# Performance work log

Hardware: AMD Instinct MI355X
Metric: run time of the kernel (lower is better)

## Reference

```python
import jax, jax.numpy as jnp
import numpy as np

EPS = 1e-5
LAMBDA_REG = 1.0
ALPHA_ENTROPY = 0.5
ALPHA_DIVERSITY = 0.5

B, N, D, K = 32, 1024, 256, 512  # batch, tokens, dim_embed, num_embed


def setup_inputs() -> dict:
    key = jax.random.key(0)
    k0, k1, k2 = jax.random.split(key, 3)
    inputs = jax.random.normal(k0, (B, N, D), dtype=jnp.float32)
    gamma = jnp.ones((D,), jnp.float32)
    beta = jnp.zeros((D,), jnp.float32)
    # keras 'uniform' initializer default: U(-0.05, 0.05)
    embed_w = jax.random.uniform(k1, (D, K), jnp.float32, -0.05, 0.05)
    # keras 'random_normal' default: stddev=0.05
    d_w = jax.random.normal(k2, (D, D), jnp.float32) * 0.05
    d_b = jnp.zeros((D,), jnp.float32)
    return {"inputs": inputs, "gamma": gamma, "beta": beta,
            "embed_w": embed_w, "d_w": d_w, "d_b": d_b}


def _project_columns_to_simplex(P_sol):
    # P_sol: (K, M); project each column onto the probability simplex.
    P_t = P_sol.T                                   # (M, K)
    sorted_P = -jnp.sort(-P_t, axis=1)              # descending
    cumsum = jnp.cumsum(sorted_P, axis=1)
    k = jnp.arange(1, K + 1, dtype=P_t.dtype)
    thresholds = (cumsum - 1.0) / k
    valid = (sorted_P > thresholds).astype(jnp.int32)
    max_idx = jnp.argmax(valid * jnp.arange(K, dtype=jnp.int32), axis=1)  # (M,)
    sel_cumsum = jnp.take_along_axis(cumsum, max_idx[:, None], axis=1)[:, 0]
    theta = (sel_cumsum - 1.0) / (max_idx.astype(P_t.dtype) + 1.0)
    return jax.nn.relu(P_t - theta[:, None]).T      # (K, M)


def _forward(inputs, gamma, beta, embed_w, d_w, d_b):
    # dense + layernorm
    x = jnp.matmul(inputs, d_w) + d_b
    mean = jnp.mean(x, axis=-1, keepdims=True)
    var = jnp.var(x, axis=-1, keepdims=True)
    x = gamma * ((x - mean) / jnp.sqrt(var + EPS)) + beta

    flat = x.reshape(-1, D)                          # (M, D)
    flat_sg = jax.lax.stop_gradient(flat)

    # hard assignment (VQ-style, on detached encodings)
    dists = (jnp.sum(flat_sg ** 2, axis=1, keepdims=True)
             + jnp.sum(embed_w ** 2, axis=0, keepdims=True)
             - 2.0 * jnp.matmul(flat_sg, embed_w))   # (M, K)
    assign = jnp.argmin(dists, axis=1)
    P_tilde = jax.nn.one_hot(assign, K, dtype=jnp.float32).T  # (K, M)

    # regularized least squares: (C^T C + lam I) P = C^T Z + lam P_tilde
    C = embed_w                                       # (D, K)
    Z = flat.T                                        # (D, M)
    A = jnp.matmul(C.T, C) + LAMBDA_REG * jnp.eye(K, dtype=jnp.float32)
    b = jnp.matmul(C.T, Z) + LAMBDA_REG * P_tilde     # (K, M)
    P_sol = jnp.linalg.solve(A, b)
    P_proj = _project_columns_to_simplex(P_sol)       # (K, M)

    out_P_proj = P_proj.T.reshape(B, N, K)

    # perplexity
    p_j = jnp.mean(out_P_proj, axis=(0, 1))
    p_j = jnp.clip(p_j, 1e-10, 1.0 - 1e-9)
    p_j = p_j / jnp.sum(p_j)
    entropy_bits = -jnp.sum(p_j * jnp.log(p_j) / jnp.log(2.0))
    perplexity = jnp.power(2.0, entropy_bits)

    Zq_flat = jnp.matmul(C, P_proj).T                 # (M, D)

    # entropy regularizer
    p_mean = jnp.mean(out_P_proj, axis=(0, 1))
    p_mn = p_mean / (jnp.sum(p_mean) + EPS)
    entropy_reg = -jnp.sum(p_mn * jnp.log(p_mn + EPS))

    # diversity loss on l2-normalized codebook columns
    norm_cb = embed_w / jnp.sqrt(jnp.maximum(jnp.sum(embed_w ** 2, axis=0, keepdims=True), 1e-12))
    sims = jnp.matmul(norm_cb.T, norm_cb)
    masked = sims * (1.0 - jnp.eye(K, dtype=jnp.float32))
    diversity_loss = jnp.mean(jax.nn.relu(masked))

    primary_loss = jnp.mean((Zq_flat - flat) ** 2)  # discrete_loss=False path
    loss = primary_loss + ALPHA_ENTROPY * entropy_reg + ALPHA_DIVERSITY * diversity_loss

    Zq = Zq_flat.reshape(B, N, D)
    return Zq, out_P_proj, loss, perplexity


def reference(inputs, gamma, beta, embed_w, d_w, d_b):
    return _forward(inputs, gamma, beta, embed_w, d_w, d_b)
```

## Files before the change

### kernel.cpp

```cpp
#include <hip/hip_runtime.h>
#include <math.h>


#define M_ 32768
#define D_ 256
#define K_ 512
#define TAU 0.006f

typedef short bf16x8 __attribute__((ext_vector_type(8)));
typedef unsigned short u16x8 __attribute__((ext_vector_type(8)));
typedef unsigned short u16x4 __attribute__((ext_vector_type(4)));
typedef float f32x4 __attribute__((ext_vector_type(4)));

#define LSTR 56

__device__ inline void split_rne(float f, unsigned short& h, unsigned short& l)
{
    unsigned int u = __float_as_uint(f);
    unsigned int uh = u + (0x7FFFu + ((u >> 16) & 1u));
    h = (unsigned short)(uh >> 16);
    float fh = __uint_as_float(((unsigned int)h) << 16);
    float r = f - fh;
    l = (unsigned short)(__float_as_uint(r) >> 16);
}

__device__ inline unsigned short rne16(float f)
{
    unsigned int u = __float_as_uint(f);
    u += 0x7FFFu + ((u >> 16) & 1u);
    return (unsigned short)(u >> 16);
}

template<int EPI>
__global__ __launch_bounds__(256)
void mfma_gemm(const unsigned short* __restrict__ Ah,
               const unsigned short* __restrict__ Bh,
               float* __restrict__ Out, int Kd, int N,
               const float* __restrict__ AinvM, const int* __restrict__ assign,
               const float* Zref, float* __restrict__ lossPart)
{
    __shared__ unsigned short sA[128*LSTR];
    __shared__ unsigned short sB[128*LSTR];
    __shared__ float red[256];
    const int tid = threadIdx.x;
    const int m0 = blockIdx.y * 128, n0 = blockIdx.x * 128;
    const int w = tid >> 6, lane = tid & 63;
    const int wr = (w & 1) * 64, wc = (w >> 1) * 64;
    const int cg = lane >> 4, cr = lane & 15;

    f32x4 acc[4][4];
    const f32x4 z4 = {0.f, 0.f, 0.f, 0.f};
#pragma unroll
    for (int i = 0; i < 4; ++i)
#pragma unroll
        for (int j = 0; j < 4; ++j) acc[i][j] = z4;

    const int sr = tid >> 1;
    const int sk = (tid & 1) * 16;
    const int soff = sr * LSTR + sk;
    const unsigned short* Agh = Ah + (size_t)(m0 + sr) * Kd + sk;
    const unsigned short* Bgh = Bh + (size_t)(n0 + sr) * Kd + sk;

    for (int kb = 0; kb < Kd; kb += 32) {
        *(u16x8*)&sA[soff]     = *(const u16x8*)(Agh + kb);
        *(u16x8*)&sA[soff + 8] = *(const u16x8*)(Agh + kb + 8);
        *(u16x8*)&sB[soff]     = *(const u16x8*)(Bgh + kb);
        *(u16x8*)&sB[soff + 8] = *(const u16x8*)(Bgh + kb + 8);
        __syncthreads();
        bf16x8 ah[4], bh[4];
#pragma unroll
        for (int f = 0; f < 4; ++f) {
            ah[f] = *(const bf16x8*)&sA[(wr + f*16 + cr) * LSTR + cg*8];
            bh[f] = *(const bf16x8*)&sB[(wc + f*16 + cr) * LSTR + cg*8];
        }
#pragma unroll
        for (int i = 0; i < 4; ++i)
#pragma unroll
            for (int j = 0; j < 4; ++j)
                acc[i][j] = __builtin_amdgcn_mfma_f32_16x16x32_bf16(ah[i], bh[j], acc[i][j], 0, 0, 0);
        __syncthreads();
    }

    if (EPI == 2) {
#pragma unroll
        for (int i = 0; i < 4; ++i) {
#pragma unroll
            for (int q = 0; q < 4; ++q) {
                const int row = m0 + wr + i*16 + cg*4 + q;
                const int am = assign[row];
                const float* Arow = AinvM + (size_t)am * K_ + n0 + wc;
#pragma unroll
                for (int j = 0; j < 4; ++j)
                    Out[(size_t)row * N + n0 + wc + j*16 + cr] =
                        acc[i][j][q] + Arow[j*16 + cr];
            }
        }
    } else {
        float lsum = 0.f;
#pragma unroll
        for (int i = 0; i < 4; ++i) {
#pragma unroll
            for (int q = 0; q < 4; ++q) {
                const int row = m0 + wr + i*16 + cg*4 + q;
#pragma unroll
                for (int j = 0; j < 4; ++j) {
                    const int col = n0 + wc + j*16 + cr;
                    const float v = acc[i][j][q];
                    const float zv = Zref[(size_t)row * N + col];
                    const float d = v - zv;
                    lsum += d * d;
                    Out[(size_t)row * N + col] = v;
                }
            }
        }
        red[tid] = lsum;
        __syncthreads();
        for (int s = 128; s > 0; s >>= 1) {
            if (tid < s) red[tid] += red[tid + s];
            __syncthreads();
        }
        if (tid == 0) lossPart[blockIdx.y * gridDim.x + blockIdx.x] = red[0];
    }
}

__global__ __launch_bounds__(256)
void score_mfma_argmin(const unsigned short* __restrict__ Zh, const unsigned short* __restrict__ Zl,
                       const unsigned short* __restrict__ Bth, const unsigned short* __restrict__ Btl,
                       const float* __restrict__ cn2, const float* __restrict__ zn2,
                       float* __restrict__ PV, float* __restrict__ PB,
                       int* __restrict__ PI)
{
    __shared__ unsigned short sAh[128*LSTR], sAl[128*LSTR];
    __shared__ unsigned short sBh[128*LSTR], sBl[128*LSTR];
    __shared__ float l1v[128][2], l2v[128][2];
    __shared__ int   liv[128][2];
    const int tid = threadIdx.x;
    const int m0 = blockIdx.y * 128, n0 = blockIdx.x * 128;
    const int w = tid >> 6, lane = tid & 63;
    const int wr = (w & 1) * 64, wc = (w >> 1) * 64;
    const int cg = lane >> 4, cr = lane & 15;

    f32x4 acc[4][4];
    const f32x4 z4 = {0.f, 0.f, 0.f, 0.f};
#pragma unroll
    for (int i = 0; i < 4; ++i)
#pragma unroll
        for (int j = 0; j < 4; ++j) acc[i][j] = z4;

    const int sr = tid >> 1;
    const int sk = (tid & 1) * 16;
    const int soff = sr * LSTR + sk;
    const unsigned short* Ah = Zh  + (size_t)(m0 + sr) * D_ + sk;
    const unsigned short* Al = Zl  + (size_t)(m0 + sr) * D_ + sk;
    const unsigned short* Bh = Bth + (size_t)(n0 + sr) * D_ + sk;
    const unsigned short* Bl = Btl + (size_t)(n0 + sr) * D_ + sk;

    for (int kb = 0; kb < D_; kb += 32) {
        *(u16x8*)&sAh[soff]     = *(const u16x8*)(Ah + kb);
        *(u16x8*)&sAh[soff + 8] = *(const u16x8*)(Ah + kb + 8);
        *(u16x8*)&sAl[soff]     = *(const u16x8*)(Al + kb);
        *(u16x8*)&sAl[soff + 8] = *(const u16x8*)(Al + kb + 8);
        *(u16x8*)&sBh[soff]     = *(const u16x8*)(Bh + kb);
        *(u16x8*)&sBh[soff + 8] = *(const u16x8*)(Bh + kb + 8);
        *(u16x8*)&sBl[soff]     = *(const u16x8*)(Bl + kb);
        *(u16x8*)&sBl[soff + 8] = *(const u16x8*)(Bl + kb + 8);
        __syncthreads();
        bf16x8 ah[4], al[4], bh[4], bl[4];
#pragma unroll
        for (int f = 0; f < 4; ++f) {
            const int ao = (wr + f*16 + cr) * LSTR + cg*8;
            ah[f] = *(const bf16x8*)&sAh[ao];
            al[f] = *(const bf16x8*)&sAl[ao];
            const int bo = (wc + f*16 + cr) * LSTR + cg*8;
            bh[f] = *(const bf16x8*)&sBh[bo];
            bl[f] = *(const bf16x8*)&sBl[bo];
        }
#pragma unroll
        for (int i = 0; i < 4; ++i)
#pragma unroll
            for (int j = 0; j < 4; ++j) {
                acc[i][j] = __builtin_amdgcn_mfma_f32_16x16x32_bf16(ah[i], bh[j], acc[i][j], 0, 0, 0);
                acc[i][j] = __builtin_amdgcn_mfma_f32_16x16x32_bf16(al[i], bh[j], acc[i][j], 0, 0, 0);
                acc[i][j] = __builtin_amdgcn_mfma_f32_16x16x32_bf16(ah[i], bl[j], acc[i][j], 0, 0, 0);
            }
        __syncthreads();
    }

    const int half = wc >> 6;
#pragma unroll
    for (int i = 0; i < 4; ++i) {
#pragma unroll
        for (int q = 0; q < 4; ++q) {
            const int rl = wr + i*16 + cg*4 + q;
            const float zr = zn2[m0 + rl];
            float b1 = 3.4e38f, b2 = 3.4e38f; int i1 = 0x7fffffff;
#pragma unroll
            for (int j = 0; j < 4; ++j) {
                const int col = n0 + wc + j*16 + cr;
                const float d = (zr + cn2[col]) - 2.0f * acc[i][j][q];
                if (d < b1 || (d == b1 && col < i1)) { b2 = b1; b1 = d; i1 = col; }
                else if (d < b2) b2 = d;
            }
#pragma unroll
            for (int off = 1; off < 16; off <<= 1) {
                const float o1 = __shfl_xor(b1, off);
                const int   oi = __shfl_xor(i1, off);
                const float o2 = __shfl_xor(b2, off);
                if (o1 < b1 || (o1 == b1 && oi < i1)) { b2 = fminf(b1, o2); b1 = o1; i1 = oi; }
                else { b2 = fminf(o1, b2); }
            }
            if (cr == 0) { l1v[rl][half] = b1; l2v[rl][half] = b2; liv[rl][half] = i1; }
        }
    }
    __syncthreads();
    if (tid < 128) {
        const float a1 = l1v[tid][0], a2 = l2v[tid][0]; const int ai = liv[tid][0];
        const float c1 = l1v[tid][1], c2 = l2v[tid][1]; const int ci = liv[tid][1];
        float b1, b2; int bi;
        if (c1 < a1 || (c1 == a1 && ci < ai)) { b1 = c1; bi = ci; b2 = fminf(a1, c2); }
        else { b1 = a1; bi = ai; b2 = fminf(c1, a2); }
        const size_t o = (size_t)(m0 + tid) * 4 + blockIdx.x;
        PV[o] = b1; PB[o] = b2; PI[o] = bi;
    }
}

__global__ void argmin_reduce4(const float* __restrict__ PV, const float* __restrict__ PB,
                               const int* __restrict__ PI, int* __restrict__ assign,
                               int* __restrict__ rlist, int* __restrict__ rcount)
{
    const int m = blockIdx.x * 256 + threadIdx.x;
    float b1 = PV[(size_t)m*4], b2 = PB[(size_t)m*4]; int i1 = PI[(size_t)m*4];
#pragma unroll
    for (int s = 1; s < 4; ++s) {
        const float o1 = PV[(size_t)m*4+s], o2 = PB[(size_t)m*4+s];
        const int oi = PI[(size_t)m*4+s];
        if (o1 < b1 || (o1 == b1 && oi < i1)) { b2 = fminf(b1, o2); b1 = o1; i1 = oi; }
        else { b2 = fminf(o1, b2); }
    }
    assign[m] = i1;
    if (b2 - b1 < TAU) { const int p = atomicAdd(rcount, 1); rlist[p] = m; }
}

__global__ __launch_bounds__(256)
void repair_gemm(const float* __restrict__ Z, const float* __restrict__ B,
                 const float* __restrict__ cn2, const float* __restrict__ zn2,
                 const int* __restrict__ rlist, const int* __restrict__ rcount,
                 float* __restrict__ PV, int* __restrict__ PI)
{
    const int n = rcount[0];
    const int m0 = blockIdx.y * 128;
    if (m0 >= n) return;
    __shared__ float As[16][132];
    __shared__ float Bs[16][128];
    __shared__ int rows_s[128];
    const int tid = threadIdx.x;
    const int tx = tid & 15, ty = tid >> 4;
    const int n0 = blockIdx.x * 128;

    if (tid < 128) rows_s[tid] = (m0 + tid < n) ? rlist[m0 + tid] : rlist[0];
    __syncthreads();

    float acc[8][8];
#pragma unroll
    for (int i = 0; i < 8; ++i)
#pragma unroll
        for (int j = 0; j < 8; ++j) acc[i][j] = 0.f;

    const int ar = tid >> 1, ac = (tid & 1) * 8;
    const int br = tid >> 4, bc = (tid & 15) * 8;
    const float* Ap = Z + (size_t)rows_s[ar] * D_ + ac;
    const float* Bp = B + (size_t)br * K_ + n0 + bc;

    for (int kb = 0; kb < D_; kb += 16) {
        float4 a0 = *(const float4*)(Ap + kb);
        float4 a1 = *(const float4*)(Ap + kb + 4);
        float4 b0 = *(const float4*)(Bp + (size_t)kb * K_);
        float4 b1 = *(const float4*)(Bp + (size_t)kb * K_ + 4);
        As[ac+0][ar] = a0.x; As[ac+1][ar] = a0.y; As[ac+2][ar] = a0.z; As[ac+3][ar] = a0.w;
        As[ac+4][ar] = a1.x; As[ac+5][ar] = a1.y; As[ac+6][ar] = a1.z; As[ac+7][ar] = a1.w;
        *(float4*)&Bs[br][bc]     = b0;
        *(float4*)&Bs[br][bc + 4] = b1;
        __syncthreads();
#pragma unroll
        for (int kk = 0; kk < 16; ++kk) {
            float4 av0 = *(const float4*)&As[kk][ty*4];
            float4 av1 = *(const float4*)&As[kk][64 + ty*4];
            float4 bv0 = *(const float4*)&Bs[kk][tx*4];
            float4 bv1 = *(const float4*)&Bs[kk][64 + tx*4];
            float a_[8] = {av0.x, av0.y, av0.z, av0.w, av1.x, av1.y, av1.z, av1.w};
            float b_[8] = {bv0.x, bv0.y, bv0.z, bv0.w, bv1.x, bv1.y, bv1.z, bv1.w};
#pragma unroll
            for (int i = 0; i < 8; ++i)
#pragma unroll
                for (int j = 0; j < 8; ++j)
                    acc[i][j] = fmaf(a_[i], b_[j], acc[i][j]);
        }
        __syncthreads();
    }

#pragma unroll
    for (int hi = 0; hi < 2; ++hi) {
#pragma unroll
        for (int i = 0; i < 4; ++i) {
            const int rl = hi*64 + ty*4 + i;
            if (m0 + rl >= n) continue;
            const float zr = zn2[rows_s[rl]];
            float best = 3.4e38f; int bi = 0x7fffffff;
#pragma unroll
            for (int hj = 0; hj < 2; ++hj) {
#pragma unroll
                for (int j = 0; j < 4; ++j) {
                    const int col = n0 + hj*64 + tx*4 + j;
                    const float t1 = zr + cn2[col];
                    const float d  = t1 - 2.0f * acc[hi*4+i][hj*4+j];
                    if (d < best) { best = d; bi = col; }
                }
            }
#pragma unroll
            for (int off = 1; off < 16; off <<= 1) {
                const float ov = __shfl_xor(best, off);
                const int   oi = __shfl_xor(bi, off);
                if (ov < best || (ov == best && oi < bi)) { best = ov; bi = oi; }
            }
            if (tx == 0) {
                PV[(size_t)(m0 + rl) * 4 + blockIdx.x] = best;
                PI[(size_t)(m0 + rl) * 4 + blockIdx.x] = bi;
            }
        }
    }
}

__global__ void repair_scatter(const float* __restrict__ PV, const int* __restrict__ PI,
                               const int* __restrict__ rlist, const int* __restrict__ rcount,
                               int* __restrict__ assign)
{
    const int r = blockIdx.x * 256 + threadIdx.x;
    if (r >= rcount[0]) return;
    float best = PV[(size_t)r * 4]; int bi = PI[(size_t)r * 4];
#pragma unroll
    for (int nb = 1; nb < 4; ++nb) {
        const float v = PV[(size_t)r * 4 + nb]; const int ix = PI[(size_t)r * 4 + nb];
        if (v < best || (v == best && ix < bi)) { best = v; bi = ix; }
    }
    assign[rlist[r]] = bi;
}

__global__ __launch_bounds__(512)
void dense_ln_kernel(const float* __restrict__ A, const float* __restrict__ Bw,
                     const float* __restrict__ bias, const float* __restrict__ gamma,
                     const float* __restrict__ beta, float* __restrict__ Z,
                     float* __restrict__ zn2,
                     unsigned short* __restrict__ Zh, unsigned short* __restrict__ Zl)
{
    __shared__ float As[16][68];
    __shared__ float Bs[16][260];
    __shared__ float rred[64][17];
    __shared__ float rstat[64];
    const int tid = threadIdx.x, tx = tid & 15, ty = tid >> 4;
    const int m0 = blockIdx.x * 64;
    float acc[2][16];
#pragma unroll
    for (int i = 0; i < 2; ++i)
#pragma unroll
        for (int j = 0; j < 16; ++j) acc[i][j] = 0.f;

    const int ar = tid >> 3, ac = (tid & 7) * 2;
    const int br = tid >> 5, bc = (tid & 31) * 8;
    for (int kb = 0; kb < 256; kb += 16) {
        {
            float2 a = *(const float2*)(A + (size_t)(m0 + ar) * 256 + kb + ac);
            As[ac][ar] = a.x; As[ac + 1][ar] = a.y;
            *(float4*)&Bs[br][bc]     = *(const float4*)(Bw + (size_t)(kb + br) * 256 + bc);
            *(float4*)&Bs[br][bc + 4] = *(const float4*)(Bw + (size_t)(kb + br) * 256 + bc + 4);
        }
        __syncthreads();
#pragma unroll
        for (int kk = 0; kk < 16; ++kk) {
            float av[2] = {As[kk][ty*2], As[kk][ty*2 + 1]};
            float bv[16];
#pragma unroll
            for (int q = 0; q < 4; ++q) {
                float4 b4 = *(const float4*)&Bs[kk][q*64 + tx*4];
                bv[q*4+0] = b4.x; bv[q*4+1] = b4.y; bv[q*4+2] = b4.z; bv[q*4+3] = b4.w;
            }
#pragma unroll
            for (int i = 0; i < 2; ++i)
#pragma unroll
                for (int j = 0; j < 16; ++j)
                    acc[i][j] = fmaf(av[i], bv[j], acc[i][j]);
        }
        __syncthreads();
    }

    float bcol[16];
#pragma unroll
    for (int q = 0; q < 4; ++q) {
        float4 b4 = *(const float4*)(bias + q*64 + tx*4);
        bcol[q*4+0] = b4.x; bcol[q*4+1] = b4.y; bcol[q*4+2] = b4.z; bcol[q*4+3] = b4.w;
    }
#pragma unroll
    for (int i = 0; i < 2; ++i)
#pragma unroll
        for (int j = 0; j < 16; ++j) acc[i][j] += bcol[j];

#pragma unroll
    for (int i = 0; i < 2; ++i) {
        float s = 0.f;
#pragma unroll
        for (int j = 0; j < 16; ++j) s += acc[i][j];
        rred[ty*2+i][tx] = s;
    }
    __syncthreads();
    if (tid < 64) {
        float s = 0.f;
#pragma unroll
        for (int t = 0; t < 16; ++t) s += rred[tid][t];
        rstat[tid] = s * (1.f / 256.f);
    }
    __syncthreads();
    float mean_[2];
#pragma unroll
    for (int i = 0; i < 2; ++i) mean_[i] = rstat[ty*2+i];

#pragma unroll
    for (int i = 0; i < 2; ++i) {
        float s = 0.f;
#pragma unroll
        for (int j = 0; j < 16; ++j) { float d = acc[i][j] - mean_[i]; s += d * d; }
        rred[ty*2+i][tx] = s;
    }
    __syncthreads();
    if (tid < 64) {
        float s = 0.f;
#pragma unroll
        for (int t = 0; t < 16; ++t) s += rred[tid][t];
        rstat[tid] = s * (1.f / 256.f);
    }
    __syncthreads();
    float rstd_[2];
#pragma unroll
    for (int i = 0; i < 2; ++i) rstd_[i] = sqrtf(rstat[ty*2+i] + 1e-5f);

    float gam[16], bet[16];
#pragma unroll
    for (int q = 0; q < 4; ++q) {
        float4 g4 = *(const float4*)(gamma + q*64 + tx*4);
        float4 e4 = *(const float4*)(beta  + q*64 + tx*4);
        gam[q*4+0] = g4.x; gam[q*4+1] = g4.y; gam[q*4+2] = g4.z; gam[q*4+3] = g4.w;
        bet[q*4+0] = e4.x; bet[q*4+1] = e4.y; bet[q*4+2] = e4.z; bet[q*4+3] = e4.w;
    }
#pragma unroll
    for (int i = 0; i < 2; ++i)
#pragma unroll
        for (int j = 0; j < 16; ++j) {
            const float d = acc[i][j] - mean_[i];
            acc[i][j] = gam[j] * (d / rstd_[i]) + bet[j];
        }

#pragma unroll
    for (int i = 0; i < 2; ++i) {
        float s = 0.f;
#pragma unroll
        for (int j = 0; j < 16; ++j) s += acc[i][j] * acc[i][j];
        rred[ty*2+i][tx] = s;
    }
    __syncthreads();
    if (tid < 64) {
        float s = 0.f;
#pragma unroll
        for (int t = 0; t < 16; ++t) s += rred[tid][t];
        zn2[m0 + tid] = s;
    }

#pragma unroll
    for (int i = 0; i < 2; ++i) {
        const int row = m0 + ty*2 + i;
#pragma unroll
        for (int q = 0; q < 4; ++q) {
            float4 v;
            v.x = acc[i][q*4+0]; v.y = acc[i][q*4+1];
            v.z = acc[i][q*4+2]; v.w = acc[i][q*4+3];
            const size_t pos = (size_t)row * 256 + q*64 + tx*4;
            *(float4*)(Z + pos) = v;
            unsigned short h[4], l[4];
            split_rne(v.x, h[0], l[0]); split_rne(v.y, h[1], l[1]);
            split_rne(v.z, h[2], l[2]); split_rne(v.w, h[3], l[3]);
            *(u16x4*)(Zh + pos) = *(u16x4*)h;
            *(u16x4*)(Zl + pos) = *(u16x4*)l;
        }
    }
}

template<int TRA, int ASUM, int BSUM, int OEPI>
__global__ __launch_bounds__(256)
void sk_gemm(const float* __restrict__ A, const float* __restrict__ B,
             float* __restrict__ Out, int M, int N, int Kd,
             const float* __restrict__ Xprev)
{
    __shared__ float As[16][68];
    __shared__ float Bs[16][68];
    const int tid = threadIdx.x;
    const int tx = tid & 15, ty = tid >> 4;
    const int n0 = blockIdx.x * 64, m0 = blockIdx.y * 64;
    const int kw = Kd >> 2;
    const int kb0 = blockIdx.z * kw;
    const size_t aP = (size_t)M * Kd;
    const size_t bP = (size_t)Kd * N;
    float acc[4][4];
#pragma unroll
    for (int i = 0; i < 4; ++i)
#pragma unroll
        for (int j = 0; j < 4; ++j) acc[i][j] = 0.f;

    for (int kb = kb0; kb < kb0 + kw; kb += 16) {
        if (TRA == 0) {
            const int ar2 = tid >> 2, ac2 = (tid & 3) * 4;
            const size_t off = (size_t)(m0 + ar2) * Kd + kb + ac2;
            float4 a;
            if (ASUM) {
                float4 a0 = *(const float4*)(A + off);
                float4 a1 = *(const float4*)(A + aP + off);
                float4 a2 = *(const float4*)(A + 2*aP + off);
                float4 a3 = *(const float4*)(A + 3*aP + off);
                a.x = a0.x + a1.x + a2.x + a3.x;
                a.y = a0.y + a1.y + a2.y + a3.y;
                a.z = a0.z + a1.z + a2.z + a3.z;
                a.w = a0.w + a1.w + a2.w + a3.w;
                if (ASUM == 2) {
                    const int row = m0 + ar2, colb = kb + ac2;
                    if (row == colb)     a.x += 1.f;
                    if (row == colb + 1) a.y += 1.f;
                    if (row == colb + 2) a.z += 1.f;
                    if (row == colb + 3) a.w += 1.f;
                }
            } else {
                a = *(const float4*)(A + off);
            }
            As[ac2+0][ar2] = a.x; As[ac2+1][ar2] = a.y;
            As[ac2+2][ar2] = a.z; As[ac2+3][ar2] = a.w;
        } else {
            const int ar2 = tid >> 4, ac2 = (tid & 15) * 4;
            float4 a = *(const float4*)(A + (size_t)(kb + ar2) * M + m0 + ac2);
            *(float4*)&As[ar2][ac2] = a;
        }
        {
            const int br2 = tid >> 4, bc2 = (tid & 15) * 4;
            const size_t off = (size_t)(kb + br2) * N + n0 + bc2;
            float4 b;
            if (BSUM) {
                float4 b0 = *(const float4*)(B + off);
                float4 b1 = *(const float4*)(B + bP + off);
                float4 b2 = *(const float4*)(B + 2*bP + off);
                float4 b3 = *(const float4*)(B + 3*bP + off);
                b.x = b0.x + b1.x + b2.x + b3.x;
                b.y = b0.y + b1.y + b2.y + b3.y;
                b.z = b0.z + b1.z + b2.z + b3.z;
                b.w = b0.w + b1.w + b2.w + b3.w;
            } else {
                b = *(const float4*)(B + off);
            }
            *(float4*)&Bs[br2][bc2] = b;
        }
        __syncthreads();
#pragma unroll
        for (int kk = 0; kk < 16; ++kk) {
            float4 a4 = *(const float4*)&As[kk][ty*4];
            float4 b4 = *(const float4*)&Bs[kk][tx*4];
            float a_[4] = {a4.x, a4.y, a4.z, a4.w};
            float b_[4] = {b4.x, b4.y, b4.z, b4.w};
#pragma unroll
            for (int i = 0; i < 4; ++i)
#pragma unroll
                for (int j = 0; j < 4; ++j)
                    acc[i][j] = fmaf(a_[i], b_[j], acc[i][j]);
        }
        __syncthreads();
    }
    const size_t MN = (size_t)M * N;
    float* Op = Out + (size_t)blockIdx.z * MN;
#pragma unroll
    for (int i = 0; i < 4; ++i)
#pragma unroll
        for (int j = 0; j < 4; ++j) {
            const size_t idx = (size_t)(m0 + ty*4 + i) * N + n0 + tx*4 + j;
            if (OEPI == 0) {
                Op[idx] = acc[i][j];
            } else {
                float base = 0.f;
                if (blockIdx.z == 0)
                    base = 2.f * (Xprev[idx] + Xprev[MN + idx] +
                                  Xprev[2*MN + idx] + Xprev[3*MN + idx]);
                Op[idx] = base - acc[i][j];
            }
        }
}

__global__ __launch_bounds__(256)
void prep_c(const float* __restrict__ C, float* __restrict__ Ct,
            unsigned short* __restrict__ Cth, unsigned short* __restrict__ Ctl,
            unsigned short* __restrict__ Ch, float* __restrict__ cn2,
            int* __restrict__ rcount)
{
    __shared__ float red[256];
    const int k = blockIdx.x, t = threadIdx.x;
    const float v = C[(size_t)t * K_ + k];
    Ct[k * 256 + t] = v;
    unsigned short h, l;
    split_rne(v, h, l);
    Cth[k * 256 + t] = h;
    Ctl[k * 256 + t] = l;
    Ch[(size_t)t * K_ + k] = h;
    red[t] = v * v;
    __syncthreads();
    for (int s = 128; s > 0; s >>= 1) { if (t < s) red[t] += red[t + s]; __syncthreads(); }
    if (t == 0) {
        cn2[k] = red[0];
        if (k == 0) rcount[0] = 0;
    }
}

__global__ void rowabs_kernel(const float* __restrict__ Sp, float* __restrict__ rowAbs)
{
    __shared__ float red[256];
    const int r = blockIdx.x, t = threadIdx.x;
    const int idx = r * 256 + t;
    float v = Sp[idx] + Sp[65536 + idx] + Sp[131072 + idx] + Sp[196608 + idx];
    if (r == t) v += 1.f;
    red[t] = fabsf(v); __syncthreads();
    for (int s = 128; s > 0; s >>= 1) {
        if (t < s) red[t] += red[t + s];
        __syncthreads();
    }
    if (t == 0) rowAbs[r] = red[0];
}

__global__ void x1_init(const float* __restrict__ rowAbs, const float* __restrict__ Sp,
                        float* __restrict__ Xp)
{
    __shared__ float red[256];
    const int t = threadIdx.x;
    red[t] = rowAbs[t]; __syncthreads();
    for (int s = 128; s > 0; s >>= 1) {
        if (t < s) red[t] = fmaxf(red[t], red[t + s]);
        __syncthreads();
    }
    const float c = 2.f / (1.f + red[0]);
    const int idx = blockIdx.x * 256 + t;
    const int i = idx >> 8, j = idx & 255;
    float s4 = Sp[idx] + Sp[65536 + idx] + Sp[131072 + idx] + Sp[196608 + idx];
    if (i == j) s4 += 1.f;
    const float tt = c * s4;
    const float xp = c * tt;
    Xp[idx] = ((i == j) ? 2.f * c : 0.f) - xp;
    Xp[65536 + idx]  = 0.f;
    Xp[131072 + idx] = 0.f;
    Xp[196608 + idx] = 0.f;
}

__global__ __launch_bounds__(256)
void gut_reduce(const float* __restrict__ Up, unsigned short* __restrict__ Uth,
                const float* __restrict__ Gp, const float* __restrict__ cn2,
                float* __restrict__ divPart,
                const float* __restrict__ Ap, float* __restrict__ Ainv)
{
    __shared__ float red[256];
    __shared__ float rsn[512];
    const int b = blockIdx.x, t = threadIdx.x;
    if (b < 512) {
        const int idx = b * 256 + t;
        Uth[idx] = rne16(Up[idx] + Up[131072 + idx] + Up[262144 + idx] + Up[393216 + idx]);
        return;
    }
    if (b >= 768) {
        const int idx = (b - 768) * 256 + t;
        const int i = idx >> 9, j = idx & 511;
        const float s = Ap[idx] + Ap[262144 + idx] + Ap[524288 + idx] + Ap[786432 + idx];
        Ainv[idx] = ((i == j) ? 1.f : 0.f) - s;
        return;
    }
    const int gb = b - 512;
    rsn[t]       = 1.f / sqrtf(fmaxf(cn2[t], 1e-12f));
    rsn[t + 256] = 1.f / sqrtf(fmaxf(cn2[t + 256], 1e-12f));
    __syncthreads();
    float dsum = 0.f;
#pragma unroll
    for (int e = 0; e < 4; ++e) {
        const int idx = gb * 1024 + e * 256 + t;
        const int i = idx >> 9, j = idx & 511;
        const float g = Gp[idx] + Gp[262144 + idx] + Gp[524288 + idx] + Gp[786432 + idx];
        if (i != j) dsum += fmaxf(g * rsn[i] * rsn[j], 0.f);
    }
    red[t] = dsum; __syncthreads();
    for (int s = 128; s > 0; s >>= 1) {
        if (t < s) red[t] += red[t + s];
        __syncthreads();
    }
    if (t == 0) divPart[gb] = red[0];
}

__global__ __launch_bounds__(1024)
void project_colsum_kernel(float* P, unsigned short* __restrict__ Ph,
                           float* __restrict__ part)
{
    __shared__ float ps[16][512];
    const int wave = threadIdx.x >> 6;
    const int lane = threadIdx.x & 63;
    float psum[8];
#pragma unroll
    for (int j = 0; j < 8; ++j) psum[j] = 0.f;

    for (int r = 0; r < 8; ++r) {
        const int row = blockIdx.x * 128 + wave * 8 + r;
        const size_t base = (size_t)row * K_ + lane;
        float v[8];
#pragma unroll
        for (int j = 0; j < 8; ++j) v[j] = P[base + j * 64];

        float s = 0.f;
#pragma unroll
        for (int j = 0; j < 8; ++j) s += v[j];
        for (int off = 32; off > 0; off >>= 1) s += __shfl_xor(s, off);

        float theta = (s - 1.f) * (1.f / 512.f);
        int cnt = K_;
        for (int it = 0; it < K_; ++it) {
            float ls = 0.f; int lc = 0;
#pragma unroll
            for (int j = 0; j < 8; ++j)
                if (v[j] > theta) { ls += v[j]; ++lc; }
            for (int off = 32; off > 0; off >>= 1) {
                ls += __shfl_xor(ls, off);
                lc += __shfl_xor(lc, off);
            }
            if (lc == cnt) break;
            theta = (ls - 1.f) / (float)lc;
            cnt = lc;
        }
#pragma unroll
        for (int j = 0; j < 8; ++j) {
            const float o = fmaxf(v[j] - theta, 0.f);
            P[base + j * 64] = o;
            Ph[base + j * 64] = rne16(o);
            psum[j] += o;
        }
    }
#pragma unroll
    for (int j = 0; j < 8; ++j) ps[wave][lane + j * 64] = psum[j];
    __syncthreads();
    for (int c = threadIdx.x; c < 512; c += 1024) {
        float s = 0.f;
#pragma unroll
        for (int wv = 0; wv < 16; ++wv) s += ps[wv][c];
        part[(size_t)blockIdx.x * K_ + c] = s;
    }
}

__global__ __launch_bounds__(512)
void part_reduce(const float* __restrict__ part, float* __restrict__ part2)
{
    const int t = threadIdx.x, b = blockIdx.x;
    float s = 0.f;
    for (int r = 0; r < 16; ++r) s += part[(size_t)(b * 16 + r) * K_ + t];
    part2[(size_t)b * K_ + t] = s;
}

#define BLOCK_REDUCE_512(val, result) \
    red[t] = (val); __syncthreads(); \
    for (int s_ = 256; s_ > 0; s_ >>= 1) { if (t < s_) red[t] += red[t + s_]; __syncthreads(); } \
    result = red[0]; __syncthreads();

__global__ __launch_bounds__(512)
void finalize_kernel(const float* __restrict__ part2, const float* __restrict__ divPart,
                     const float* __restrict__ lossPart, float* __restrict__ out_scal)
{
    __shared__ float red[512];
    const int t = threadIdx.x;

    float praw = 0.f;
    for (int b = 0; b < 16; ++b) praw += part2[b * K_ + t];
    const float pm = praw * (1.f / 32768.f);

    const float pj = fminf(fmaxf(pm, 1e-10f), 1.0f);
    float sp; BLOCK_REDUCE_512(pj, sp);
    const float pjn = pj / sp;
    float Hbits; BLOCK_REDUCE_512(-pjn * logf(pjn) / 0.69314718056f, Hbits);

    float spm; BLOCK_REDUCE_512(pm, spm);
    const float s2 = spm + 1e-5f;
    const float pmn = pm / s2;
    float ereg; BLOCK_REDUCE_512(-pmn * logf(pmn + 1e-5f), ereg);

    float dv = (t < 256) ? divPart[t] : 0.f;
    float divs; BLOCK_REDUCE_512(dv, divs);
    const float divloss = divs * (1.f / 262144.f);

    float lp = lossPart[t];
    float prim; BLOCK_REDUCE_512(lp, prim);
    prim *= 1.f / 8388608.f;

    if (t == 0) {
        out_scal[0] = prim + 0.5f * ereg + 0.5f * divloss;
        out_scal[1] = exp2f(Hbits);
    }
}

extern "C" void kernel_launch(void* const* d_in, const int* in_sizes, int n_in,
                              void* d_out, int out_size, void* d_ws, size_t ws_size,
                              hipStream_t stream)
{
    const float* inputs = (const float*)d_in[0];
    const float* gamma  = (const float*)d_in[1];
    const float* beta   = (const float*)d_in[2];
    const float* C      = (const float*)d_in[3];
    const float* d_w    = (const float*)d_in[4];
    const float* d_b    = (const float*)d_in[5];

    float* out = (float*)d_out;
    float* Z = out;
    float* P = out + (size_t)M_ * D_;
    float* out_scal = P + (size_t)M_ * K_;

    float* w = (float*)d_ws;
    float* Sp   = w;     w += 4 * 65536;
    float* Tp   = w;     w += 4 * 65536;
    float* XpA  = w;     w += 4 * 65536;
    float* XpB  = w;     w += 4 * 65536;
    float* Up   = w;     w += 4 * 131072;
    float* Ap   = w;     w += 4 * 262144;
    float* Gp   = w;     w += 4 * 262144;
    float* Ainv = w;     w += 262144;
    float* Ct   = w;     w += 131072;
    float* cn2  = w;     w += 512;
    float* rowAbs = w;   w += 256;
    float* zn2  = w;     w += M_;
    float* part = w;     w += 256 * K_;
    float* part2 = w;    w += 16 * K_;
    float* lossPart = w; w += 512;
    float* divPart  = w; w += 256;
    float* PV   = w;     w += M_ * 4;
    float* PB   = w;     w += M_ * 4;
    int* PI     = (int*)w; w += M_ * 4;
    int* rlist  = (int*)w; w += M_;
    int* rcount = (int*)w; w += 16;
    int* assign = (int*)w; w += M_;
    unsigned short* Zh  = (unsigned short*)w; w += M_ * D_ / 2;
    unsigned short* Zl  = (unsigned short*)w; w += M_ * D_ / 2;
    unsigned short* Cth = (unsigned short*)w; w += (K_ * D_) / 2;
    unsigned short* Ctl = (unsigned short*)w; w += (K_ * D_) / 2;
    unsigned short* Ch  = (unsigned short*)w; w += (K_ * D_) / 2;
    unsigned short* Uth = (unsigned short*)w; w += (K_ * D_) / 2;
    unsigned short* Ph  = Zh;

    dense_ln_kernel<<<M_/64, 512, 0, stream>>>(inputs, d_w, d_b, gamma, beta, Z, zn2, Zh, Zl);
    prep_c<<<K_, 256, 0, stream>>>(C, Ct, Cth, Ctl, Ch, cn2, rcount);
    sk_gemm<1, 0, 0, 0><<<dim3(4, 4, 4), 256, 0, stream>>>(Ct, Ct, Sp, 256, 256, 512, nullptr);
    rowabs_kernel<<<256, 256, 0, stream>>>(Sp, rowAbs);
    x1_init<<<256, 256, 0, stream>>>(rowAbs, Sp, XpA);
    float* Xc = XpA; float* Xn = XpB;
    for (int it = 0; it < 3; ++it) {
        sk_gemm<0, 2, 1, 0><<<dim3(4, 4, 4), 256, 0, stream>>>(Sp, Xc, Tp, 256, 256, 256, nullptr);
        sk_gemm<0, 1, 1, 1><<<dim3(4, 4, 4), 256, 0, stream>>>(Xc, Tp, Xn, 256, 256, 256, Xc);
        float* tmp = Xc; Xc = Xn; Xn = tmp;
    }
    sk_gemm<1, 0, 1, 0><<<dim3(4, 8, 4), 256, 0, stream>>>(C, Xc, Up, 512, 256, 256, nullptr);
    sk_gemm<0, 1, 0, 0><<<dim3(8, 8, 4), 256, 0, stream>>>(Up, C, Ap, 512, 512, 256, nullptr);
    sk_gemm<1, 0, 0, 0><<<dim3(8, 8, 4), 256, 0, stream>>>(C, C, Gp, 512, 512, 256, nullptr);
    gut_reduce<<<1792, 256, 0, stream>>>(Up, Uth, Gp, cn2, divPart, Ap, Ainv);
    score_mfma_argmin<<<dim3(K_/128, M_/128), 256, 0, stream>>>(Zh, Zl, Cth, Ctl, cn2, zn2, PV, PB, PI);
    argmin_reduce4<<<M_/256, 256, 0, stream>>>(PV, PB, PI, assign, rlist, rcount);
    repair_gemm<<<dim3(4, M_/128), 256, 0, stream>>>(Z, C, cn2, zn2, rlist, rcount, PV, PI);
    repair_scatter<<<M_/256, 256, 0, stream>>>(PV, PI, rlist, rcount, assign);
    mfma_gemm<2><<<dim3(K_/128, M_/128), 256, 0, stream>>>(
        Zh, Uth, P, D_, K_, Ainv, assign, nullptr, nullptr);
    project_colsum_kernel<<<M_/128, 1024, 0, stream>>>(P, Ph, part);
    part_reduce<<<16, 512, 0, stream>>>(part, part2);
    mfma_gemm<3><<<dim3(D_/128, M_/128), 256, 0, stream>>>(
        Ph, Ch, Z, K_, D_, nullptr, nullptr, Z, lossPart);
    finalize_kernel<<<1, 512, 0, stream>>>(part2, divPart, lossPart, out_scal);

    (void)in_sizes; (void)n_in; (void)out_size; (void)ws_size;
}
```

Baseline: 389.1 us.

## Compute Gram and A-inverse with bf16 MFMA GEMMs and fused epilogues

Replaces the two split-K fp32 sk_gemm launches for the 512x512 products (U^T C and C^T C) with single-pass bf16 MFMA GEMMs. The identity-minus and cosine-diversity reductions move into new GEMM epilogues, and the combined gut_reduce kernel is reduced to a small Uth reduction. This removes split-K partial buffers and one reduction pass. In exchange these matrices are computed with single bf16 operands (hi parts only), which lowers the precision of Ainv and the diversity loss.

```diff
diff --git a/kernel.cpp b/kernel.cpp
--- a/kernel.cpp
+++ b/kernel.cpp
@@ -95,6 +95,49 @@
                         acc[i][j][q] + Arow[j*16 + cr];
             }
         }
+    } else if (EPI == 4) {
+#pragma unroll
+        for (int i = 0; i < 4; ++i) {
+#pragma unroll
+            for (int q = 0; q < 4; ++q) {
+                const int row = m0 + wr + i*16 + cg*4 + q;
+#pragma unroll
+                for (int j = 0; j < 4; ++j) {
+                    const int col = n0 + wc + j*16 + cr;
+                    Out[(size_t)row * N + col] =
+                        ((row == col) ? 1.f : 0.f) - acc[i][j][q];
+                }
+            }
+        }
+    } else if (EPI == 5) {
+        __shared__ float rsn[512];
+        if (tid < 256) {
+            rsn[tid]       = 1.f / sqrtf(fmaxf(AinvM[tid], 1e-12f));
+            rsn[tid + 256] = 1.f / sqrtf(fmaxf(AinvM[tid + 256], 1e-12f));
+        }
+        __syncthreads();
+        float dsum = 0.f;
+#pragma unroll
+        for (int i = 0; i < 4; ++i) {
+#pragma unroll
+            for (int q = 0; q < 4; ++q) {
+                const int row = m0 + wr + i*16 + cg*4 + q;
+                const float ri = rsn[row];
+#pragma unroll
+                for (int j = 0; j < 4; ++j) {
+                    const int col = n0 + wc + j*16 + cr;
+                    if (row != col)
+                        dsum += fmaxf(acc[i][j][q] * ri * rsn[col], 0.f);
+                }
+            }
+        }
+        red[tid] = dsum;
+        __syncthreads();
+        for (int s = 128; s > 0; s >>= 1) {
+            if (tid < s) red[tid] += red[tid + s];
+            __syncthreads();
+        }
+        if (tid == 0) lossPart[blockIdx.y * gridDim.x + blockIdx.x] = red[0];
     } else {
         float lsum = 0.f;
 #pragma unroll
@@ -657,45 +700,10 @@
     Xp[196608 + idx] = 0.f;
 }
 
-__global__ __launch_bounds__(256)
-void gut_reduce(const float* __restrict__ Up, unsigned short* __restrict__ Uth,
-                const float* __restrict__ Gp, const float* __restrict__ cn2,
-                float* __restrict__ divPart,
-                const float* __restrict__ Ap, float* __restrict__ Ainv)
-{
-    __shared__ float red[256];
-    __shared__ float rsn[512];
-    const int b = blockIdx.x, t = threadIdx.x;
-    if (b < 512) {
-        const int idx = b * 256 + t;
-        Uth[idx] = rne16(Up[idx] + Up[131072 + idx] + Up[262144 + idx] + Up[393216 + idx]);
-        return;
-    }
-    if (b >= 768) {
-        const int idx = (b - 768) * 256 + t;
-        const int i = idx >> 9, j = idx & 511;
-        const float s = Ap[idx] + Ap[262144 + idx] + Ap[524288 + idx] + Ap[786432 + idx];
-        Ainv[idx] = ((i == j) ? 1.f : 0.f) - s;
-        return;
-    }
-    const int gb = b - 512;
-    rsn[t]       = 1.f / sqrtf(fmaxf(cn2[t], 1e-12f));
-    rsn[t + 256] = 1.f / sqrtf(fmaxf(cn2[t + 256], 1e-12f));
-    __syncthreads();
-    float dsum = 0.f;
-#pragma unroll
-    for (int e = 0; e < 4; ++e) {
-        const int idx = gb * 1024 + e * 256 + t;
-        const int i = idx >> 9, j = idx & 511;
-        const float g = Gp[idx] + Gp[262144 + idx] + Gp[524288 + idx] + Gp[786432 + idx];
-        if (i != j) dsum += fmaxf(g * rsn[i] * rsn[j], 0.f);
-    }
-    red[t] = dsum; __syncthreads();
-    for (int s = 128; s > 0; s >>= 1) {
-        if (t < s) red[t] += red[t + s];
-        __syncthreads();
-    }
-    if (t == 0) divPart[gb] = red[0];
+__global__ void ut_reduce(const float* __restrict__ Up, unsigned short* __restrict__ Uth)
+{
+    const int idx = blockIdx.x * 256 + threadIdx.x;
+    Uth[idx] = rne16(Up[idx] + Up[131072 + idx] + Up[262144 + idx] + Up[393216 + idx]);
 }
 
 __global__ __launch_bounds__(1024)
@@ -790,7 +798,7 @@
     const float pmn = pm / s2;
     float ereg; BLOCK_REDUCE_512(-pmn * logf(pmn + 1e-5f), ereg);
 
-    float dv = (t < 256) ? divPart[t] : 0.f;
+    float dv = (t < 16) ? divPart[t] : 0.f;
     float divs; BLOCK_REDUCE_512(dv, divs);
     const float divloss = divs * (1.f / 262144.f);
 
@@ -826,8 +834,6 @@
     float* XpA  = w;     w += 4 * 65536;
     float* XpB  = w;     w += 4 * 65536;
     float* Up   = w;     w += 4 * 131072;
-    float* Ap   = w;     w += 4 * 262144;
-    float* Gp   = w;     w += 4 * 262144;
     float* Ainv = w;     w += 262144;
     float* Ct   = w;     w += 131072;
     float* cn2  = w;     w += 512;
@@ -853,6 +859,8 @@
 
     dense_ln_kernel<<<M_/64, 512, 0, stream>>>(inputs, d_w, d_b, gamma, beta, Z, zn2, Zh, Zl);
     prep_c<<<K_, 256, 0, stream>>>(C, Ct, Cth, Ctl, Ch, cn2, rcount);
+    mfma_gemm<5><<<dim3(4, 4), 256, 0, stream>>>(
+        Cth, Cth, nullptr, D_, K_, cn2, nullptr, nullptr, divPart);
     sk_gemm<1, 0, 0, 0><<<dim3(4, 4, 4), 256, 0, stream>>>(Ct, Ct, Sp, 256, 256, 512, nullptr);
     rowabs_kernel<<<256, 256, 0, stream>>>(Sp, rowAbs);
     x1_init<<<256, 256, 0, stream>>>(rowAbs, Sp, XpA);
@@ -863,9 +871,9 @@
         float* tmp = Xc; Xc = Xn; Xn = tmp;
     }
     sk_gemm<1, 0, 1, 0><<<dim3(4, 8, 4), 256, 0, stream>>>(C, Xc, Up, 512, 256, 256, nullptr);
-    sk_gemm<0, 1, 0, 0><<<dim3(8, 8, 4), 256, 0, stream>>>(Up, C, Ap, 512, 512, 256, nullptr);
-    sk_gemm<1, 0, 0, 0><<<dim3(8, 8, 4), 256, 0, stream>>>(C, C, Gp, 512, 512, 256, nullptr);
-    gut_reduce<<<1792, 256, 0, stream>>>(Up, Uth, Gp, cn2, divPart, Ap, Ainv);
+    ut_reduce<<<512, 256, 0, stream>>>(Up, Uth);
+    mfma_gemm<4><<<dim3(4, 4), 256, 0, stream>>>(
+        Uth, Cth, Ainv, D_, K_, nullptr, nullptr, nullptr, nullptr);
     score_mfma_argmin<<<dim3(K_/128, M_/128), 256, 0, stream>>>(Zh, Zl, Cth, Ctl, cn2, zn2, PV, PB, PI);
     argmin_reduce4<<<M_/256, 256, 0, stream>>>(PV, PB, PI, assign, rlist, rcount);
     repair_gemm<<<dim3(4, M_/128), 256, 0, stream>>>(Z, C, cn2, zn2, rlist, rcount, PV, PI);
```

After: 390.8 us. Within noise of the previous version (+0.4%).
